# Kernel optimization log

Hardware: AMD Instinct MI355X
Metric: run time of the kernel (lower is better)

## Reference

```python
import math
import jax, jax.numpy as jnp
import numpy as np

N_HEADS = 16

def setup_inputs() -> dict:
    key = jax.random.key(0)
    ks = jax.random.split(key, 6)
    B, T, D = 2, 4096, 1024
    m, dh = 256, D // N_HEADS
    x = jax.random.normal(ks[0], (B, T, D), dtype=jnp.float32)
    s = 1.0 / math.sqrt(D)
    wq = jax.random.normal(ks[1], (D, D), dtype=jnp.float32) * s
    wk = jax.random.normal(ks[2], (D, D), dtype=jnp.float32) * s
    wv = jax.random.normal(ks[3], (D, D), dtype=jnp.float32) * s
    wo = jax.random.normal(ks[4], (D, D), dtype=jnp.float32) * s
    rf = jax.random.normal(ks[5], (m, dh), dtype=jnp.float32) / math.sqrt(dh)
    return {"x": x, "wq": wq, "wk": wk, "wv": wv, "wo": wo, "rf": rf}

def _phi(x, rf, m):
    # x: [B,H,T,Dh]; rf: [m,Dh] -> phi: [B,H,T,2m]
    norms_sq = jnp.sum(x * x, axis=-1, keepdims=True)            # [B,H,T,1]
    proj = jnp.einsum('bhtd,md->bhtm', x, rf)                     # [B,H,T,m]
    scale = jnp.exp(-norms_sq * 0.5) / math.sqrt(m)
    return jnp.concatenate([jnp.cos(proj), jnp.sin(proj)], axis=-1) * scale

def reference(x, wq, wk, wv, wo, rf):
    B, T, D = x.shape
    H = N_HEADS
    Dh = D // H
    m = rf.shape[0]
    def heads(w):
        return (x @ w.T).reshape(B, T, H, Dh).transpose(0, 2, 1, 3)  # [B,H,T,Dh]
    Q, K, V = heads(wq), heads(wk), heads(wv)
    Qf = _phi(Q, rf, m)                                            # [B,H,T,2m]
    Kf = _phi(K, rf, m)
    KV = jnp.einsum('bhnd,bhnv->bhdv', Kf, V)                      # [B,H,2m,Dh]
    QKV = jnp.einsum('bhnd,bhdv->bhnv', Qf, KV)                    # [B,H,T,Dh]
    K_sum = jnp.sum(Kf, axis=2)                                    # [B,H,2m]
    Z = jnp.maximum(jnp.einsum('bhnd,bhd->bhn', Qf, K_sum)[..., None], 1e-6)
    out = (QKV / Z).transpose(0, 2, 1, 3).reshape(B, T, D)
    return out @ wo.T
```

## Files before the change

### kernel.cpp

```cpp
#include <hip/hip_runtime.h>


#define TSEQ  4096
#define BSZ   2
#define BT    8192
#define DM    1024
#define NHEAD 16
#define DHEAD 64
#define FF    512

typedef __attribute__((ext_vector_type(8))) __bf16 bf16x8;
typedef __attribute__((ext_vector_type(4))) __bf16 bf16x4;
typedef __attribute__((ext_vector_type(4))) float floatx4;

#define MFMA_BF16(a, b, c) __builtin_amdgcn_mfma_f32_16x16x32_bf16(a, b, c, 0, 0, 0)

__device__ __forceinline__ void load_lds_16B(const void* g, void* l) {
    __builtin_amdgcn_global_load_lds(
        (const __attribute__((address_space(1))) void*)g,
        (__attribute__((address_space(3))) void*)l, 16, 0, 0);
}

__global__ __launch_bounds__(256) void split2_kernel(
    const float* __restrict__ src, __bf16* __restrict__ hi, __bf16* __restrict__ lo, int n4)
{
    int i = blockIdx.x * 256 + threadIdx.x;
    if (i >= n4) return;
    float4 v = ((const float4*)src)[i];
    bf16x4 h = {(__bf16)v.x, (__bf16)v.y, (__bf16)v.z, (__bf16)v.w};
    bf16x4 l = {(__bf16)(v.x - (float)h[0]), (__bf16)(v.y - (float)h[1]),
                (__bf16)(v.z - (float)h[2]), (__bf16)(v.w - (float)h[3])};
    ((bf16x4*)hi)[i] = h;
    ((bf16x4*)lo)[i] = l;
}

__global__ __launch_bounds__(256) void split_weights_kernel(
    const float* __restrict__ wq, const float* __restrict__ wk,
    const float* __restrict__ wv, const float* __restrict__ wo,
    const float* __restrict__ rf,
    __bf16* __restrict__ Wqh, __bf16* __restrict__ Wql,
    __bf16* __restrict__ Wkh, __bf16* __restrict__ Wkl,
    __bf16* __restrict__ Wvh, __bf16* __restrict__ Woh,
    __bf16* __restrict__ rfh, __bf16* __restrict__ rfl)
{
    const int id = blockIdx.x;
    const float* src; __bf16* dh; __bf16* dl; int i;
    if (id < 1024)      { src = wq; dh = Wqh; dl = Wql;     i = id * 256; }
    else if (id < 2048) { src = wk; dh = Wkh; dl = Wkl;     i = (id - 1024) * 256; }
    else if (id < 3072) { src = wv; dh = Wvh; dl = nullptr; i = (id - 2048) * 256; }
    else if (id < 4096) { src = wo; dh = Woh; dl = nullptr; i = (id - 3072) * 256; }
    else                { src = rf; dh = rfh; dl = rfl;     i = (id - 4096) * 256; }
    i += threadIdx.x;
    float4 v = ((const float4*)src)[i];
    bf16x4 h = {(__bf16)v.x, (__bf16)v.y, (__bf16)v.z, (__bf16)v.w};
    ((bf16x4*)dh)[i] = h;
    if (dl) {
        bf16x4 l = {(__bf16)(v.x - (float)h[0]), (__bf16)(v.y - (float)h[1]),
                    (__bf16)(v.z - (float)h[2]), (__bf16)(v.w - (float)h[3])};
        ((bf16x4*)dl)[i] = l;
    }
}

__global__ __launch_bounds__(512, 4)
void gemm_qk_kernel(const __bf16* __restrict__ Ahi, const __bf16* __restrict__ Alo,
                    const __bf16* __restrict__ Wqh, const __bf16* __restrict__ Wql,
                    const __bf16* __restrict__ Wkh, const __bf16* __restrict__ Wkl,
                    __bf16* __restrict__ Qb, __bf16* __restrict__ Kb,
                    float* __restrict__ Qnorm, float* __restrict__ Knorm)
{
    __shared__ __bf16 As[2][4096];
    __shared__ __bf16 Bq[2][4096];
    __shared__ __bf16 Bk[2][4096];

    const int t = threadIdx.x;
    const int bm = blockIdx.x * 128, bn = blockIdx.y * 128;
    const int lane = t & 63, mth = lane & 15, q = lane >> 4;
    const int wave = t >> 6, grp = wave >> 2, wv = wave & 3;
    const int wrow = (wv & 1) * 64, wcol = (wv >> 1) * 64;
    const int qsw = q ^ ((mth >> 1) & 3);
    const int row = t >> 2;
    const int csw = (t & 3) ^ ((row >> 1) & 3);

    const size_t arow = (size_t)(bm + row) * DM + csw * 8;
    const size_t brow = (size_t)(bn + row) * DM + csw * 8;

    floatx4 acc[4][4];
#pragma unroll
    for (int i = 0; i < 4; ++i)
#pragma unroll
        for (int j = 0; j < 4; ++j) acc[i][j] = (floatx4){0.f, 0.f, 0.f, 0.f};

    const char* Bbase = grp ? (const char*)Bk : (const char*)Bq;

    for (int k0 = 0; k0 < DM; k0 += 32) {
        __syncthreads();
        load_lds_16B(Ahi + arow + k0, (char*)As + t * 16);
        load_lds_16B(Alo + arow + k0, (char*)As + 8192 + t * 16);
        load_lds_16B(Wqh + brow + k0, (char*)Bq + t * 16);
        load_lds_16B(Wql + brow + k0, (char*)Bq + 8192 + t * 16);
        load_lds_16B(Wkh + brow + k0, (char*)Bk + t * 16);
        load_lds_16B(Wkl + brow + k0, (char*)Bk + 8192 + t * 16);
        __syncthreads();

        bf16x8 ah[4], al[4];
#pragma unroll
        for (int i = 0; i < 4; ++i) {
            const int ao = ((wrow + i * 16 + mth) * 32 + qsw * 8) * 2;
            ah[i] = *(const bf16x8*)((const char*)As + ao);
            al[i] = *(const bf16x8*)((const char*)As + 8192 + ao);
        }
#pragma unroll
        for (int j = 0; j < 4; ++j) {
            const int bo = ((wcol + j * 16 + mth) * 32 + qsw * 8) * 2;
            const bf16x8 bh = *(const bf16x8*)(Bbase + bo);
            const bf16x8 bl = *(const bf16x8*)(Bbase + 8192 + bo);
#pragma unroll
            for (int i = 0; i < 4; ++i) {
                acc[i][j] = MFMA_BF16(ah[i], bh, acc[i][j]);
                acc[i][j] = MFMA_BF16(ah[i], bl, acc[i][j]);
                acc[i][j] = MFMA_BF16(al[i], bh, acc[i][j]);
            }
        }
    }

    __bf16* Cb = grp ? Kb : Qb;
    float* norms = grp ? Knorm : Qnorm;
    const int head = (bn + wcol) >> 6;
#pragma unroll
    for (int i = 0; i < 4; ++i)
#pragma unroll
        for (int r = 0; r < 4; ++r) {
            float s = acc[i][0][r] * acc[i][0][r] + acc[i][1][r] * acc[i][1][r]
                    + acc[i][2][r] * acc[i][2][r] + acc[i][3][r] * acc[i][3][r];
            s += __shfl_xor(s, 1); s += __shfl_xor(s, 2);
            s += __shfl_xor(s, 4); s += __shfl_xor(s, 8);
            const int grow = bm + wrow + i * 16 + q * 4 + r;
            if (mth == 0) norms[(size_t)head * BT + grow] = s;
            const size_t gr = (size_t)grow * DM + bn + wcol + mth;
#pragma unroll
            for (int j = 0; j < 4; ++j) Cb[gr + j * 16] = (__bf16)acc[i][j][r];
        }
}

template<int EPI>
__global__ __launch_bounds__(256, 2)
void gemm_mfma_kernel(const __bf16* __restrict__ Ahi, const __bf16* __restrict__ Whi,
                      float* __restrict__ Cf, __bf16* __restrict__ Cb)
{
    __shared__ __bf16 As[4096];
    __shared__ __bf16 Bs[4096];
    __shared__ __bf16 TrS[EPI == 3 ? 4 * 64 * 66 : 1];

    const int t = threadIdx.x;
    const int bm = blockIdx.x * 128, bn = blockIdx.y * 128;
    const int lane = t & 63, mth = lane & 15, q = lane >> 4, wave = t >> 6;
    const int wrow = (wave & 1) * 64, wcol = (wave >> 1) * 64;
    const int qsw = q ^ ((mth >> 1) & 3);
    const int row = t >> 2;
    const int csw = (t & 3) ^ ((row >> 1) & 3);

    const size_t arow = (size_t)(bm + (t >> 2)) * DM + csw * 8;
    const size_t brow = (size_t)(bn + (t >> 2)) * DM + csw * 8;
    const int l0 = t * 8;
    const int l1 = 64 * 32 + t * 8;

    floatx4 acc[4][4];
#pragma unroll
    for (int i = 0; i < 4; ++i)
#pragma unroll
        for (int j = 0; j < 4; ++j) acc[i][j] = (floatx4){0.f, 0.f, 0.f, 0.f};

    for (int k0 = 0; k0 < DM; k0 += 32) {
        __syncthreads();
        load_lds_16B(Ahi + arow + k0,           &As[l0]);
        load_lds_16B(Ahi + arow + 64 * DM + k0, &As[l1]);
        load_lds_16B(Whi + brow + k0,           &Bs[l0]);
        load_lds_16B(Whi + brow + 64 * DM + k0, &Bs[l1]);
        __syncthreads();

        bf16x8 ah[4], bh[4];
#pragma unroll
        for (int i = 0; i < 4; ++i) {
            ah[i] = *(const bf16x8*)&As[(wrow + i * 16 + mth) * 32 + qsw * 8];
            bh[i] = *(const bf16x8*)&Bs[(wcol + i * 16 + mth) * 32 + qsw * 8];
        }
#pragma unroll
        for (int i = 0; i < 4; ++i)
#pragma unroll
            for (int j = 0; j < 4; ++j)
                acc[i][j] = MFMA_BF16(ah[i], bh[j], acc[i][j]);
    }

    if (EPI == 3) {
        __bf16* Tr = TrS + wave * (64 * 66);
#pragma unroll
        for (int i = 0; i < 4; ++i)
#pragma unroll
            for (int j = 0; j < 4; ++j) {
                bf16x4 w = {(__bf16)acc[i][j][0], (__bf16)acc[i][j][1],
                            (__bf16)acc[i][j][2], (__bf16)acc[i][j][3]};
                *(bf16x4*)(Tr + (j * 16 + mth) * 66 + i * 16 + q * 4) = w;
            }
        const int cg = bn + wcol + lane;
        const int hh = cg >> 6, vloc = cg & 63;
        const int r0 = bm + wrow;
        const int bb = r0 >> 12, tloc = r0 & 4095;
        __bf16* dst = Cb + ((size_t)(bb * 16 + hh) * 64 + vloc) * TSEQ + tloc;
#pragma unroll
        for (int k = 0; k < 8; ++k)
            *(bf16x8*)(dst + k * 8) = *(const bf16x8*)(Tr + lane * 66 + k * 8);
        return;
    }
#pragma unroll
    for (int i = 0; i < 4; ++i)
#pragma unroll
        for (int r = 0; r < 4; ++r) {
            const size_t gr = (size_t)(bm + wrow + i * 16 + q * 4 + r) * DM
                            + bn + wcol + mth;
#pragma unroll
            for (int j = 0; j < 4; ++j) Cf[gr + j * 16] = acc[i][j][r];
        }
}

__global__ __launch_bounds__(256, 3)
void kv_mfma_kernel(const __bf16* __restrict__ Kb, const __bf16* __restrict__ Vt,
                    const float* __restrict__ Knorm,
                    const __bf16* __restrict__ rfh_g, const __bf16* __restrict__ rfl_g,
                    float* __restrict__ KVpart)
{
    __shared__ __bf16 rfh[4096], rfl[4096], Kc[4096], VtS[5120], phiT[8192];
    __shared__ float scaleS[64];

    const int fb = blockIdx.x, bh = blockIdx.y, z = blockIdx.z;
    const int b = bh >> 4, h = bh & 15;
    const int tid = threadIdx.x, wave = tid >> 6, lane = tid & 63;
    const int m = lane & 15, q = lane >> 4;
    const int lr = lane >> 2;
    const int csw = (lane & 3) ^ ((lr >> 1) & 3);
    const int qsw = q ^ ((m >> 1) & 3);

#pragma unroll
    for (int L = 0; L < 2; ++L) {
        const int f = wave * 16 + lr, d = L * 32 + csw * 8;
        load_lds_16B(rfh_g + (size_t)(fb * 64 + f) * DHEAD + d,
                     (char*)rfh + L * 4096 + wave * 1024 + lane * 16);
        load_lds_16B(rfl_g + (size_t)(fb * 64 + f) * DHEAD + d,
                     (char*)rfl + L * 4096 + wave * 1024 + lane * 16);
    }
    for (int idx = tid; idx < 1024; idx += 256) {
        const int kt = idx >> 9, rr = (idx >> 5) & 15, cc = idx & 31;
        VtS[kt * 2560 + (64 + rr) * 32 + cc] = (rr == 0) ? (__bf16)1.0f : (__bf16)0.0f;
    }

    floatx4 acc[2][5];
#pragma unroll
    for (int s = 0; s < 2; ++s)
#pragma unroll
        for (int v = 0; v < 5; ++v) acc[s][v] = (floatx4){0.f, 0.f, 0.f, 0.f};

    for (int ch = z * 8; ch < z * 8 + 8; ++ch) {
        __syncthreads();
#pragma unroll
        for (int L = 0; L < 2; ++L) {
            const int tr = wave * 16 + lr, d = L * 32 + csw * 8;
            load_lds_16B(Kb + (size_t)(b * TSEQ + ch * 64 + tr) * DM + h * 64 + d,
                         (char*)Kc + L * 4096 + wave * 1024 + lane * 16);
            load_lds_16B(Vt + ((size_t)bh * 64 + tr) * TSEQ + ch * 64 + d,
                         (char*)VtS + L * 5120 + wave * 1024 + lane * 16);
        }
        if (tid < 64)
            scaleS[tid] = __expf(-0.5f * Knorm[(size_t)h * BT + b * TSEQ + ch * 64 + tid]) * 0.0625f;
        __syncthreads();

        floatx4 pr[4];
#pragma unroll
        for (int ft = 0; ft < 4; ++ft) pr[ft] = (floatx4){0.f, 0.f, 0.f, 0.f};
#pragma unroll
        for (int kt = 0; kt < 2; ++kt) {
            const bf16x8 ka = *(const bf16x8*)(Kc + kt * 2048 + (wave * 16 + m) * 32 + qsw * 8);
#pragma unroll
            for (int ft = 0; ft < 4; ++ft) {
                const bf16x8 yh = *(const bf16x8*)(rfh + kt * 2048 + (ft * 16 + m) * 32 + qsw * 8);
                const bf16x8 yl = *(const bf16x8*)(rfl + kt * 2048 + (ft * 16 + m) * 32 + qsw * 8);
                pr[ft] = MFMA_BF16(ka, yh, pr[ft]);
                pr[ft] = MFMA_BF16(ka, yl, pr[ft]);
            }
        }
        {
            const int pg = wave >> 1;
            const int cph = (wave & 1) * 2 + (q >> 1);
            const int sub8 = (q & 1) * 8;
#pragma unroll
            for (int ft = 0; ft < 4; ++ft) {
                const int fo = ft * 16 + m;
                bf16x4 pc, ps;
#pragma unroll
                for (int r = 0; r < 4; ++r) {
                    const float sc = scaleS[wave * 16 + q * 4 + r];
                    float sv, cv;
                    __sincosf(pr[ft][r], &sv, &cv);
                    pc[r] = (__bf16)(cv * sc);
                    ps[r] = (__bf16)(sv * sc);
                }
                const int off = pg * 8192 + fo * 64 + (cph ^ ((m >> 1) & 3)) * 16 + sub8;
                *(bf16x4*)((char*)phiT + off) = pc;
                *(bf16x4*)((char*)phiT + off + 4096) = ps;
            }
        }
        __syncthreads();

#pragma unroll
        for (int kt = 0; kt < 2; ++kt) {
            bf16x8 yph[2];
#pragma unroll
            for (int f2 = 0; f2 < 2; ++f2)
                yph[f2] = *(const bf16x8*)((char*)phiT + kt * 8192
                          + (wave * 32 + f2 * 16 + m) * 64 + qsw * 16);
#pragma unroll
            for (int vt = 0; vt < 5; ++vt) {
                const bf16x8 xv = *(const bf16x8*)(VtS + kt * 2560 + (vt * 16 + m) * 32 + qsw * 8);
#pragma unroll
                for (int f2 = 0; f2 < 2; ++f2)
                    acc[f2][vt] = MFMA_BF16(xv, yph[f2], acc[f2][vt]);
            }
        }
    }

#pragma unroll
    for (int f2 = 0; f2 < 2; ++f2) {
        const int fo = wave * 32 + f2 * 16 + m;
        const int fg = (fo < 64) ? fb * 64 + fo : 256 + fb * 64 + (fo - 64);
#pragma unroll
        for (int vt = 0; vt < 5; ++vt) {
            float* base = KVpart + ((size_t)(z * 32 + bh) * 80 + vt * 16 + q * 4) * 512 + fg;
#pragma unroll
            for (int r = 0; r < 4; ++r) base[(size_t)r * 512] = acc[f2][vt][r];
        }
    }
}

#define KVTN (32 * 80 * 512)

__global__ __launch_bounds__(256) void reduce_kv_kernel(
    const float* __restrict__ KVpart, __bf16* __restrict__ KVthi)
{
    const int i = blockIdx.x * 256 + threadIdx.x;
    const float4* P = (const float4*)KVpart;
    float4 s = P[i];
#pragma unroll
    for (int j = 1; j < 8; ++j) {
        const float4 p = P[i + (size_t)j * (KVTN / 4)];
        s.x += p.x; s.y += p.y; s.z += p.z; s.w += p.w;
    }
    bf16x4 hv = {(__bf16)s.x, (__bf16)s.y, (__bf16)s.z, (__bf16)s.w};
    ((bf16x4*)KVthi)[i] = hv;
}

__global__ __launch_bounds__(256, 3)
void qkv_mfma_kernel(const __bf16* __restrict__ Qb, const float* __restrict__ Qnorm,
                     const __bf16* __restrict__ rfh_g, const __bf16* __restrict__ rfl_g,
                     const __bf16* __restrict__ KVthi, __bf16* __restrict__ Ybf)
{
    __shared__ __bf16 Qs[8192];
    __shared__ __bf16 uS[8192];
    __shared__ __bf16 uS2[8192];
    __shared__ __bf16 KVh[10240];
    __shared__ float scaleS[128];

    const int tt = blockIdx.x, bh = blockIdx.y;
    const int b = bh >> 4, h = bh & 15;
    const int t0 = tt * 128;
    const int tid = threadIdx.x, wave = tid >> 6, lane = tid & 63;
    const int m = lane & 15, q = lane >> 4;
    const int lr = lane >> 2;
    const int cswl = (lane & 3) ^ ((lr >> 1) & 3);
    const int qsw = q ^ ((m >> 1) & 3);
    const int trq = tid >> 2;
    const int cswq = (tid & 3) ^ ((trq >> 1) & 3);

    if (tid < 128)
        scaleS[tid] = __expf(-0.5f * Qnorm[(size_t)h * BT + b * TSEQ + t0 + tid]) * 0.0625f;

#pragma unroll
    for (int p = 0; p < 4; ++p) {
        const int sub = p >> 1, kt = p & 1;
        load_lds_16B(Qb + (size_t)(b * TSEQ + t0 + sub * 64 + trq) * DM + h * 64
                        + kt * 32 + cswq * 8,
                     (char*)Qs + p * 4096 + tid * 16);
    }

    floatx4 acc[2][5];
#pragma unroll
    for (int s = 0; s < 2; ++s)
#pragma unroll
        for (int v = 0; v < 5; ++v) acc[s][v] = (floatx4){0.f, 0.f, 0.f, 0.f};

    for (int fb = 0; fb < 4; ++fb) {
        __syncthreads();
#pragma unroll
        for (int p = 0; p < 2; ++p) {
            load_lds_16B(rfh_g + (size_t)(fb * 64 + trq) * DHEAD + p * 32 + cswq * 8,
                         (char*)uS + p * 4096 + tid * 16);
            load_lds_16B(rfl_g + (size_t)(fb * 64 + trq) * DHEAD + p * 32 + cswq * 8,
                         (char*)uS2 + p * 4096 + tid * 16);
        }
        {
            const int fgb = (wave < 2) ? fb * 64 + wave * 32 : 256 + fb * 64 + (wave - 2) * 32;
#pragma unroll
            for (int L = 0; L < 5; ++L) {
                const int v = L * 16 + lr;
                load_lds_16B(KVthi + ((size_t)bh * 80 + v) * 512 + fgb + cswl * 8,
                             (char*)KVh + wave * 5120 + L * 1024 + lane * 16);
            }
        }
        __syncthreads();

        floatx4 pr[2][4];
#pragma unroll
        for (int s = 0; s < 2; ++s)
#pragma unroll
            for (int i = 0; i < 4; ++i) pr[s][i] = (floatx4){0.f, 0.f, 0.f, 0.f};
#pragma unroll
        for (int kt = 0; kt < 2; ++kt) {
            const int xo = kt * 4096 + ((wave * 16 + m) * 32 + qsw * 8) * 2;
            const bf16x8 xh = *(const bf16x8*)((const char*)uS + xo);
            const bf16x8 xl = *(const bf16x8*)((const char*)uS2 + xo);
#pragma unroll
            for (int sub = 0; sub < 2; ++sub)
#pragma unroll
                for (int tt_ = 0; tt_ < 4; ++tt_) {
                    const bf16x8 yq = *(const bf16x8*)((const char*)Qs + (sub * 2 + kt) * 4096
                                      + ((tt_ * 16 + m) * 32 + qsw * 8) * 2);
                    pr[sub][tt_] = MFMA_BF16(xh, yq, pr[sub][tt_]);
                    pr[sub][tt_] = MFMA_BF16(xl, yq, pr[sub][tt_]);
                }
        }
        __syncthreads();

#pragma unroll
        for (int sub = 0; sub < 2; ++sub) {
            {
                const int pg = wave >> 1;
                const int cph = (wave & 1) * 2 + (q >> 1);
                const int sub8 = (q & 1) * 8;
#pragma unroll
                for (int tt_ = 0; tt_ < 4; ++tt_) {
                    const int tloc = tt_ * 16 + m;
                    const float sc = scaleS[sub * 64 + tloc];
                    bf16x4 pc, ps;
#pragma unroll
                    for (int r = 0; r < 4; ++r) {
                        float sv, cv;
                        __sincosf(pr[sub][tt_][r], &sv, &cv);
                        pc[r] = (__bf16)(cv * sc);
                        ps[r] = (__bf16)(sv * sc);
                    }
                    const int off = pg * 4096 + tloc * 64 + (cph ^ ((m >> 1) & 3)) * 16 + sub8;
                    *(bf16x4*)((char*)uS + off) = pc;
                    *(bf16x4*)((char*)uS2 + off) = ps;
                }
            }
            __syncthreads();

#pragma unroll
            for (int ktf = 0; ktf < 4; ++ktf) {
                const char* phip = (ktf < 2) ? (const char*)uS + ktf * 4096
                                             : (const char*)uS2 + (ktf - 2) * 4096;
                const bf16x8 yf = *(const bf16x8*)(phip + (wave * 16 + m) * 64 + qsw * 16);
#pragma unroll
                for (int vt = 0; vt < 5; ++vt) {
                    const bf16x8 xh = *(const bf16x8*)(KVh + ktf * 2560 + (vt * 16 + m) * 32 + qsw * 8);
                    acc[sub][vt] = MFMA_BF16(xh, yf, acc[sub][vt]);
                }
            }
            if (sub == 0) __syncthreads();
        }
    }
#pragma unroll
    for (int sub = 0; sub < 2; ++sub) {
        const float zv = __shfl(acc[sub][4][0], m);
        const float inv = 1.0f / fmaxf(zv, 1e-6f);
        const size_t tg = (size_t)(b * TSEQ + t0 + sub * 64 + wave * 16 + m);
#pragma unroll
        for (int vt = 0; vt < 4; ++vt) {
            bf16x4 w;
#pragma unroll
            for (int r = 0; r < 4; ++r) w[r] = (__bf16)(acc[sub][vt][r] * inv);
            *(bf16x4*)(Ybf + tg * DM + h * 64 + vt * 16 + q * 4) = w;
        }
    }
}

extern "C" void kernel_launch(void* const* d_in, const int* in_sizes, int n_in,
                              void* d_out, int out_size, void* d_ws, size_t ws_size,
                              hipStream_t stream)
{
    (void)in_sizes; (void)n_in; (void)out_size; (void)ws_size;
    const float* x  = (const float*)d_in[0];
    const float* wq = (const float*)d_in[1];
    const float* wk = (const float*)d_in[2];
    const float* wv = (const float*)d_in[3];
    const float* wo = (const float*)d_in[4];
    const float* rf = (const float*)d_in[5];
    float* out = (float*)d_out;

    const size_t MN = (size_t)BT * DM;
    const size_t WN = (size_t)DM * DM;
    const size_t RN = 256 * 64;

    __bf16* Qb    = (__bf16*)d_ws;
    __bf16* Kbf   = Qb   + MN;
    __bf16* Vtb   = Kbf  + MN;
    __bf16* Xhi   = Vtb  + MN;
    __bf16* Xlo   = Xhi  + MN;
    __bf16* Wqh   = Xlo  + MN;
    __bf16* Wql   = Wqh + WN;
    __bf16* Wkh   = Wql + WN;
    __bf16* Wkl   = Wkh + WN;
    __bf16* Wvh   = Wkl + WN;
    __bf16* Woh   = Wvh + WN;
    __bf16* rfhb  = Woh + WN;
    __bf16* rflb  = rfhb + RN;
    float* Qnorm  = (float*)(rflb + RN);
    float* Knorm  = Qnorm + (size_t)BT * NHEAD;
    __bf16* KVthi = (__bf16*)(Knorm + (size_t)BT * NHEAD);
    float* KVpart = (float*)Xhi;
    __bf16* Ybf   = Xhi;

    const dim3 blk(256);
    hipLaunchKernelGGL(split2_kernel, dim3(MN / 4 / 256), blk, 0, stream,
                       x, Xhi, Xlo, (int)(MN / 4));
    hipLaunchKernelGGL(split_weights_kernel, dim3(4096 + RN / 4 / 256), blk, 0, stream,
                       wq, wk, wv, wo, rf, Wqh, Wql, Wkh, Wkl, Wvh, Woh, rfhb, rflb);

    hipLaunchKernelGGL(gemm_qk_kernel, dim3(64, 8), dim3(512), 0, stream,
                       Xhi, Xlo, Wqh, Wql, Wkh, Wkl, Qb, Kbf, Qnorm, Knorm);
    hipLaunchKernelGGL((gemm_mfma_kernel<3>), dim3(64, 8), blk, 0, stream,
                       Xhi, Wvh, (float*)nullptr, Vtb);

    hipLaunchKernelGGL(kv_mfma_kernel, dim3(4, 32, 8), blk, 0, stream,
                       Kbf, Vtb, Knorm, rfhb, rflb, KVpart);
    hipLaunchKernelGGL(reduce_kv_kernel, dim3(KVTN / 4 / 256), blk, 0, stream,
                       KVpart, KVthi);
    hipLaunchKernelGGL(qkv_mfma_kernel, dim3(32, 32), blk, 0, stream,
                       Qb, Qnorm, rfhb, rflb, KVthi, Ybf);

    hipLaunchKernelGGL((gemm_mfma_kernel<0>), dim3(64, 8), blk, 0, stream,
                       Ybf, Woh, out, (__bf16*)nullptr);
}
```

Before: 326.5 us.

## Drop low-order bf16 split for random features and merge split kernels

Removes the hi/lo bf16 split of the random-feature matrix, so the feature projection in the KV and QKV kernels uses one MFMA per tile instead of two. It also drops the extra LDS loads of the low part. The input and weight split kernels are merged into a single launch. This lowers MFMA, LDS and launch cost, but the phase of cos/sin now carries bf16 rounding error from rf, which could hurt accuracy.

```diff
diff --git a/kernel.cpp b/kernel.cpp
--- a/kernel.cpp
+++ b/kernel.cpp
@@ -21,35 +21,25 @@
         (__attribute__((address_space(3))) void*)l, 16, 0, 0);
 }
 
-__global__ __launch_bounds__(256) void split2_kernel(
-    const float* __restrict__ src, __bf16* __restrict__ hi, __bf16* __restrict__ lo, int n4)
-{
-    int i = blockIdx.x * 256 + threadIdx.x;
-    if (i >= n4) return;
-    float4 v = ((const float4*)src)[i];
-    bf16x4 h = {(__bf16)v.x, (__bf16)v.y, (__bf16)v.z, (__bf16)v.w};
-    bf16x4 l = {(__bf16)(v.x - (float)h[0]), (__bf16)(v.y - (float)h[1]),
-                (__bf16)(v.z - (float)h[2]), (__bf16)(v.w - (float)h[3])};
-    ((bf16x4*)hi)[i] = h;
-    ((bf16x4*)lo)[i] = l;
-}
-
-__global__ __launch_bounds__(256) void split_weights_kernel(
+__global__ __launch_bounds__(256) void split_all_kernel(
+    const float* __restrict__ x,
     const float* __restrict__ wq, const float* __restrict__ wk,
     const float* __restrict__ wv, const float* __restrict__ wo,
     const float* __restrict__ rf,
+    __bf16* __restrict__ Xhi, __bf16* __restrict__ Xlo,
     __bf16* __restrict__ Wqh, __bf16* __restrict__ Wql,
     __bf16* __restrict__ Wkh, __bf16* __restrict__ Wkl,
     __bf16* __restrict__ Wvh, __bf16* __restrict__ Woh,
-    __bf16* __restrict__ rfh, __bf16* __restrict__ rfl)
+    __bf16* __restrict__ rfh)
 {
     const int id = blockIdx.x;
     const float* src; __bf16* dh; __bf16* dl; int i;
-    if (id < 1024)      { src = wq; dh = Wqh; dl = Wql;     i = id * 256; }
-    else if (id < 2048) { src = wk; dh = Wkh; dl = Wkl;     i = (id - 1024) * 256; }
-    else if (id < 3072) { src = wv; dh = Wvh; dl = nullptr; i = (id - 2048) * 256; }
-    else if (id < 4096) { src = wo; dh = Woh; dl = nullptr; i = (id - 3072) * 256; }
-    else                { src = rf; dh = rfh; dl = rfl;     i = (id - 4096) * 256; }
+    if (id < 8192)       { src = x;  dh = Xhi; dl = Xlo;     i = id * 256; }
+    else if (id < 9216)  { src = wq; dh = Wqh; dl = Wql;     i = (id - 8192) * 256; }
+    else if (id < 10240) { src = wk; dh = Wkh; dl = Wkl;     i = (id - 9216) * 256; }
+    else if (id < 11264) { src = wv; dh = Wvh; dl = nullptr; i = (id - 10240) * 256; }
+    else if (id < 12288) { src = wo; dh = Woh; dl = nullptr; i = (id - 11264) * 256; }
+    else                 { src = rf; dh = rfh; dl = nullptr; i = (id - 12288) * 256; }
     i += threadIdx.x;
     float4 v = ((const float4*)src)[i];
     bf16x4 h = {(__bf16)v.x, (__bf16)v.y, (__bf16)v.z, (__bf16)v.w};
@@ -225,10 +215,10 @@
 __global__ __launch_bounds__(256, 3)
 void kv_mfma_kernel(const __bf16* __restrict__ Kb, const __bf16* __restrict__ Vt,
                     const float* __restrict__ Knorm,
-                    const __bf16* __restrict__ rfh_g, const __bf16* __restrict__ rfl_g,
+                    const __bf16* __restrict__ rfh_g,
                     float* __restrict__ KVpart)
 {
-    __shared__ __bf16 rfh[4096], rfl[4096], Kc[4096], VtS[5120], phiT[8192];
+    __shared__ __bf16 rfh[4096], Kc[4096], VtS[5120], phiT[8192];
     __shared__ float scaleS[64];
 
     const int fb = blockIdx.x, bh = blockIdx.y, z = blockIdx.z;
@@ -244,8 +234,6 @@
         const int f = wave * 16 + lr, d = L * 32 + csw * 8;
         load_lds_16B(rfh_g + (size_t)(fb * 64 + f) * DHEAD + d,
                      (char*)rfh + L * 4096 + wave * 1024 + lane * 16);
-        load_lds_16B(rfl_g + (size_t)(fb * 64 + f) * DHEAD + d,
-                     (char*)rfl + L * 4096 + wave * 1024 + lane * 16);
     }
     for (int idx = tid; idx < 1024; idx += 256) {
         const int kt = idx >> 9, rr = (idx >> 5) & 15, cc = idx & 31;
@@ -281,9 +269,7 @@
 #pragma unroll
             for (int ft = 0; ft < 4; ++ft) {
                 const bf16x8 yh = *(const bf16x8*)(rfh + kt * 2048 + (ft * 16 + m) * 32 + qsw * 8);
-                const bf16x8 yl = *(const bf16x8*)(rfl + kt * 2048 + (ft * 16 + m) * 32 + qsw * 8);
                 pr[ft] = MFMA_BF16(ka, yh, pr[ft]);
-                pr[ft] = MFMA_BF16(ka, yl, pr[ft]);
             }
         }
         {
@@ -358,7 +344,7 @@
 
 __global__ __launch_bounds__(256, 3)
 void qkv_mfma_kernel(const __bf16* __restrict__ Qb, const float* __restrict__ Qnorm,
-                     const __bf16* __restrict__ rfh_g, const __bf16* __restrict__ rfl_g,
+                     const __bf16* __restrict__ rfh_g,
                      const __bf16* __restrict__ KVthi, __bf16* __restrict__ Ybf)
 {
     __shared__ __bf16 Qs[8192];
@@ -401,8 +387,6 @@
         for (int p = 0; p < 2; ++p) {
             load_lds_16B(rfh_g + (size_t)(fb * 64 + trq) * DHEAD + p * 32 + cswq * 8,
                          (char*)uS + p * 4096 + tid * 16);
-            load_lds_16B(rfl_g + (size_t)(fb * 64 + trq) * DHEAD + p * 32 + cswq * 8,
-                         (char*)uS2 + p * 4096 + tid * 16);
         }
         {
             const int fgb = (wave < 2) ? fb * 64 + wave * 32 : 256 + fb * 64 + (wave - 2) * 32;
@@ -424,7 +408,6 @@
         for (int kt = 0; kt < 2; ++kt) {
             const int xo = kt * 4096 + ((wave * 16 + m) * 32 + qsw * 8) * 2;
             const bf16x8 xh = *(const bf16x8*)((const char*)uS + xo);
-            const bf16x8 xl = *(const bf16x8*)((const char*)uS2 + xo);
 #pragma unroll
             for (int sub = 0; sub < 2; ++sub)
 #pragma unroll
@@ -432,7 +415,6 @@
                     const bf16x8 yq = *(const bf16x8*)((const char*)Qs + (sub * 2 + kt) * 4096
                                       + ((tt_ * 16 + m) * 32 + qsw * 8) * 2);
                     pr[sub][tt_] = MFMA_BF16(xh, yq, pr[sub][tt_]);
-                    pr[sub][tt_] = MFMA_BF16(xl, yq, pr[sub][tt_]);
                 }
         }
         __syncthreads();
@@ -520,18 +502,16 @@
     __bf16* Wvh   = Wkl + WN;
     __bf16* Woh   = Wvh + WN;
     __bf16* rfhb  = Woh + WN;
-    __bf16* rflb  = rfhb + RN;
-    float* Qnorm  = (float*)(rflb + RN);
+    float* Qnorm  = (float*)(rfhb + RN);
     float* Knorm  = Qnorm + (size_t)BT * NHEAD;
     __bf16* KVthi = (__bf16*)(Knorm + (size_t)BT * NHEAD);
     float* KVpart = (float*)Xhi;
     __bf16* Ybf   = Xhi;
 
     const dim3 blk(256);
-    hipLaunchKernelGGL(split2_kernel, dim3(MN / 4 / 256), blk, 0, stream,
-                       x, Xhi, Xlo, (int)(MN / 4));
-    hipLaunchKernelGGL(split_weights_kernel, dim3(4096 + RN / 4 / 256), blk, 0, stream,
-                       wq, wk, wv, wo, rf, Wqh, Wql, Wkh, Wkl, Wvh, Woh, rfhb, rflb);
+    hipLaunchKernelGGL(split_all_kernel, dim3(12304), blk, 0, stream,
+                       x, wq, wk, wv, wo, rf,
+                       Xhi, Xlo, Wqh, Wql, Wkh, Wkl, Wvh, Woh, rfhb);
 
     hipLaunchKernelGGL(gemm_qk_kernel, dim3(64, 8), dim3(512), 0, stream,
                        Xhi, Xlo, Wqh, Wql, Wkh, Wkl, Qb, Kbf, Qnorm, Knorm);
@@ -539,11 +519,11 @@
                        Xhi, Wvh, (float*)nullptr, Vtb);
 
     hipLaunchKernelGGL(kv_mfma_kernel, dim3(4, 32, 8), blk, 0, stream,
-                       Kbf, Vtb, Knorm, rfhb, rflb, KVpart);
+                       Kbf, Vtb, Knorm, rfhb, KVpart);
     hipLaunchKernelGGL(reduce_kv_kernel, dim3(KVTN / 4 / 256), blk, 0, stream,
                        KVpart, KVthi);
     hipLaunchKernelGGL(qkv_mfma_kernel, dim3(32, 32), blk, 0, stream,
-                       Qb, Qnorm, rfhb, rflb, KVthi, Ybf);
+                       Qb, Qnorm, rfhb, KVthi, Ybf);
 
     hipLaunchKernelGGL((gemm_mfma_kernel<0>), dim3(64, 8), blk, 0, stream,
                        Ybf, Woh, out, (__bf16*)nullptr);
```

After: 320.1 us. About the same (-1.9%).
